# Kernel tuning notes

Measured on AMD Instinct MI355X. Metric: run time of the kernel, lower is better.

The kernel has to match this reference:

```python
import jax, jax.numpy as jnp
import numpy as np

N, X_DIM, Y_DIM, HID = 8192, 512, 2048 // 4, 2048
Y_DIM = 512

def setup_inputs() -> dict:
    key = jax.random.key(0)
    ks = jax.random.split(key, 10)
    def lin(k, fan_in, fan_out):
        lim = 1.0 / np.sqrt(fan_in)
        kw, kb = jax.random.split(k)
        W = jax.random.uniform(kw, (fan_in, fan_out), jnp.float32, -lim, lim)
        b = jax.random.uniform(kb, (fan_out,), jnp.float32, -lim, lim)
        return W, b
    mu_W1, mu_b1 = lin(ks[0], X_DIM, HID)
    mu_W2, mu_b2 = lin(ks[1], HID, Y_DIM)
    lv_W1, lv_b1 = lin(ks[2], X_DIM, HID)
    lv_W2, lv_b2 = lin(ks[3], HID, Y_DIM)
    return {
        "x_samples": jax.random.normal(ks[4], (N, X_DIM), jnp.float32),
        "y_samples": jax.random.normal(ks[5], (N, Y_DIM), jnp.float32),
        "mu_W1": mu_W1, "mu_b1": mu_b1, "mu_W2": mu_W2, "mu_b2": mu_b2,
        "lv_W1": lv_W1, "lv_b1": lv_b1, "lv_W2": lv_W2, "lv_b2": lv_b2,
    }

def reference(x_samples, y_samples, mu_W1, mu_b1, mu_W2, mu_b2, lv_W1, lv_b1, lv_W2, lv_b2):
    # MLP heads (GEMMs)
    mu = jax.nn.relu(x_samples @ mu_W1 + mu_b1) @ mu_W2 + mu_b2          # [N, D]
    logvar = jnp.tanh(jax.nn.relu(x_samples @ lv_W1 + lv_b1) @ lv_W2 + lv_b2)  # [N, D]
    w = 0.5 * jnp.exp(-logvar)                                           # 1/(2*exp(logvar))
    n = x_samples.shape[0]

    # positive: -mean_i sum_d (mu_id - y_id)^2 * w_id
    positive = -(((mu - y_samples) ** 2) * w).sum(axis=1).mean()

    # negative (exact decomposition of the [N,N,D] broadcast):
    # -(1/N^2) sum_{i,d} w_id * (N*mu_id^2 - 2*mu_id*Sy_d + Sy2_d)
    Sy = y_samples.sum(axis=0)          # [D]
    Sy2 = (y_samples ** 2).sum(axis=0)  # [D]
    negative = -(w * (n * mu ** 2 - 2.0 * mu * Sy + Sy2)).sum() / (n * n)

    return positive - negative
```

## Files before the change

### kernel.cpp

```cpp
#include <hip/hip_runtime.h>
#include <hip/hip_bf16.h>
#include <stdint.h>

#define NS   8192
#define XD   512
#define HD   2048
#define YD   512

typedef unsigned short u16;
using bf16x8 = __attribute__((ext_vector_type(8))) short;
using f32x4  = __attribute__((ext_vector_type(4))) float;

__device__ __forceinline__ float bf2f(u16 u) {
  union { uint32_t i; float f; } v; v.i = ((uint32_t)u) << 16; return v.f;
}
__device__ __forceinline__ u16 f2b(float f) {
  __hip_bfloat16 hb = __float2bfloat16(f);
  return *(const u16*)&hb;
}
__device__ __forceinline__ float ld_in(const void* p, int f32, size_t i) {
  return f32 ? ((const float*)p)[i] : bf2f(((const u16*)p)[i]);
}
#define GLDS(gp, lp) __builtin_amdgcn_global_load_lds( \
    (__attribute__((address_space(1))) void*)(gp),     \
    (__attribute__((address_space(3))) void*)(lp), 16, 0, 0)

__device__ __forceinline__ int probe_f32(const void* p, int n_u16, int* sflag) {
  if (threadIdx.x == 0) *sflag = 0;
  __syncthreads();
  const u16* q = (const u16*)p;
  int wild = 0;
  for (int i = threadIdx.x; i < n_u16; i += blockDim.x) {
    float v = bf2f(q[i]);
    if (!(fabsf(v) <= 1000.0f)) wild = 1;
  }
  if (wild) *sflag = 1;
  __syncthreads();
  int r = *sflag;
  __syncthreads();
  return r;
}

__global__ __launch_bounds__(256) void prep_all(
    const void* __restrict__ x,
    const void* w1m, const void* b1m, const void* w2m, const void* b2m,
    const void* w1l, const void* b1l, const void* w2l, const void* b2l,
    const void* __restrict__ y,
    u16* __restrict__ xb, float* __restrict__ biasv,
    u16* __restrict__ W1t, u16* __restrict__ W2tm, u16* __restrict__ W2tl,
    float* __restrict__ Sy, float* __restrict__ Sy2) {
  __shared__ u16 tile[64 * 72];
  __shared__ int sflag;
  const int b = blockIdx.x;
  const int tid = threadIdx.x;

  if (b < 2048) {
    if (!probe_f32(x, 1024, &sflag)) return;
    const size_t base = (size_t)b * 2048 + (size_t)tid * 8;
    alignas(16) u16 o[8];
    const float4* s = (const float4*)((const float*)x + base);
    float4 v0 = s[0], v1 = s[1];
    o[0]=f2b(v0.x); o[1]=f2b(v0.y); o[2]=f2b(v0.z); o[3]=f2b(v0.w);
    o[4]=f2b(v1.x); o[5]=f2b(v1.y); o[6]=f2b(v1.z); o[7]=f2b(v1.w);
    *(uint4*)(xb + base) = *(const uint4*)o;
  } else if (b == 2048) {
    const int f3 = probe_f32(b1m, 1024, &sflag);
    const int f5 = probe_f32(b2m, 512, &sflag);
    const int f7 = probe_f32(b1l, 1024, &sflag);
    const int f9 = probe_f32(b2l, 512, &sflag);
    for (int i = tid; i < 5120; i += 256) {
      float v;
      if (i < 2048)      v = ld_in(b1m, f3, i);
      else if (i < 4096) v = ld_in(b1l, f7, i - 2048);
      else if (i < 4608) v = ld_in(b2m, f5, i - 4096);
      else               v = ld_in(b2l, f9, i - 4608);
      biasv[i] = v;
    }
  } else if (b < 3073) {
    const int id = b - 2049, which = id >> 8, t = id & 255;
    const void* in; u16* out; int R, C;
    if (which == 0)      { in = w1m; out = W1t;                   R = XD; C = HD; }
    else if (which == 1) { in = w2m; out = W2tm;                  R = HD; C = YD; }
    else if (which == 2) { in = w1l; out = W1t + (size_t)HD * XD; R = XD; C = HD; }
    else                 { in = w2l; out = W2tl;                  R = HD; C = YD; }
    const int f = probe_f32(in, 1024, &sflag);
    const int nbx = C >> 6;
    const int c0 = (t % nbx) * 64, r0 = (t / nbx) * 64;
    const int r = tid >> 2, cc = (tid & 3) * 16;
    if (f) {
      const float4* s = (const float4*)((const float*)in + (size_t)(r0 + r) * C + c0 + cc);
#pragma unroll
      for (int k = 0; k < 4; ++k) {
        float4 v = s[k];
        tile[r * 72 + cc + k * 4 + 0] = f2b(v.x);
        tile[r * 72 + cc + k * 4 + 1] = f2b(v.y);
        tile[r * 72 + cc + k * 4 + 2] = f2b(v.z);
        tile[r * 72 + cc + k * 4 + 3] = f2b(v.w);
      }
    } else {
      const uint4* s = (const uint4*)((const u16*)in + (size_t)(r0 + r) * C + c0 + cc);
      *(uint4*)&tile[r * 72 + cc]     = s[0];
      *(uint4*)&tile[r * 72 + cc + 8] = s[1];
    }
    __syncthreads();
    const int i = tid >> 2, jc = (tid & 3) * 16;
    alignas(16) u16 o[16];
#pragma unroll
    for (int j = 0; j < 16; ++j) o[j] = tile[(jc + j) * 72 + i];
    uint4* dq = (uint4*)&out[(size_t)(c0 + i) * R + r0 + jc];
    dq[0] = ((const uint4*)o)[0];
    dq[1] = ((const uint4*)o)[1];
  } else {
    const int id2 = b - 3073;
    const int yf = probe_f32(y, 1024, &sflag);
    const int half = tid >> 7;
    const int c0 = (tid & 127) * 4;
    const int r0 = id2 * 128 + half * 64;
    float s0 = 0.f, s1 = 0.f, s2 = 0.f, s3 = 0.f;
    float q0 = 0.f, q1 = 0.f, q2 = 0.f, q3 = 0.f;
    for (int r = r0; r < r0 + 64; r += 4) {
#pragma unroll
      for (int rr = 0; rr < 4; ++rr) {
        float v0, v1, v2, v3;
        if (yf) {
          const float4 t4 = *(const float4*)((const float*)y + (size_t)(r + rr) * YD + c0);
          v0 = t4.x; v1 = t4.y; v2 = t4.z; v3 = t4.w;
        } else {
          const uint2 t2 = *(const uint2*)((const u16*)y + (size_t)(r + rr) * YD + c0);
          v0 = bf2f((u16)(t2.x & 0xffff)); v1 = bf2f((u16)(t2.x >> 16));
          v2 = bf2f((u16)(t2.y & 0xffff)); v3 = bf2f((u16)(t2.y >> 16));
        }
        s0 += v0; q0 += v0 * v0;  s1 += v1; q1 += v1 * v1;
        s2 += v2; q2 += v2 * v2;  s3 += v3; q3 += v3 * v3;
      }
    }
    atomicAdd(&Sy[c0],     s0);  atomicAdd(&Sy2[c0],     q0);
    atomicAdd(&Sy[c0 + 1], s1);  atomicAdd(&Sy2[c0 + 1], q1);
    atomicAdd(&Sy[c0 + 2], s2);  atomicAdd(&Sy2[c0 + 2], q2);
    atomicAdd(&Sy[c0 + 3], s3);  atomicAdd(&Sy2[c0 + 3], q3);
  }
}

#define SYNC_PRE do { \
  __builtin_amdgcn_sched_barrier(0); \
  __builtin_amdgcn_s_barrier(); \
  asm volatile("s_waitcnt lgkmcnt(0)" ::: "memory"); \
  __builtin_amdgcn_sched_barrier(0); \
  __builtin_amdgcn_s_setprio(1); } while (0)
#define SYNC_POST do { \
  __builtin_amdgcn_s_setprio(0); \
  __builtin_amdgcn_sched_barrier(0); \
  __builtin_amdgcn_s_barrier(); \
  __builtin_amdgcn_sched_barrier(0); } while (0)
#define VMCNT4 asm volatile("s_waitcnt vmcnt(4)" ::: "memory")
#define VMCNT0 asm volatile("s_waitcnt vmcnt(0)" ::: "memory")

#define RD_A(MH, BUF) do { \
  const u16* ab_ = &lds[((BUF)*2 + wm) * 8192]; \
  _Pragma("unroll") for (int q_ = 0; q_ < 4; ++q_) \
    _Pragma("unroll") for (int ks_ = 0; ks_ < 2; ++ks_) \
      af[q_][ks_] = *(const bf16x8*)&ab_[((MH)*64 + q_*16 + c16)*64 + (((ks_*4+quad) ^ cswz) << 3)]; \
} while (0)

#define RD_B(NH, BUF) do { \
  const u16* bb_ = &lds[32768 + ((BUF)*2 + (wn>>1)) * 8192]; \
  _Pragma("unroll") for (int p_ = 0; p_ < 2; ++p_) \
    _Pragma("unroll") for (int ks_ = 0; ks_ < 2; ++ks_) \
      bf[(NH)*2+p_][ks_] = *(const bf16x8*)&bb_[((wn&1)*64 + ((NH)*2+p_)*16 + c16)*64 + (((ks_*4+quad) ^ cswz) << 3)]; \
} while (0)

#define MM(MH, NH) do { \
  _Pragma("unroll") for (int ks_ = 0; ks_ < 2; ++ks_) \
    _Pragma("unroll") for (int q_ = 0; q_ < 4; ++q_) \
      _Pragma("unroll") for (int p_ = 0; p_ < 2; ++p_) \
        acc[(MH)*4+q_][(NH)*2+p_] = __builtin_amdgcn_mfma_f32_16x16x32_bf16( \
            af[q_][ks_], bf[(NH)*2+p_][ks_], acc[(MH)*4+q_][(NH)*2+p_], 0, 0, 0); \
} while (0)

#define ST_A(KT, HALF) do { if ((KT) < 8) { \
  u16* lb_ = &lds[(((KT)&1)*2 + (HALF))*8192 + (wid << 9)]; \
  const u16* sp_ = Aptr + (size_t)(bm0 + (HALF)*128 + (wid<<3) + srow)*512 + ((KT)<<6) + scg; \
  GLDS(sp_, lb_); GLDS(sp_ + (size_t)64*512, lb_ + 4096); } } while (0)

#define ST_B(KT, HALF) do { if ((KT) < 8) { \
  u16* lb_ = &lds[32768 + (((KT)&1)*2 + (HALF))*8192 + (wid << 9)]; \
  const u16* sp_ = W1t + (size_t)(bn0 + (HALF)*128 + (wid<<3) + srow)*512 + ((KT)<<6) + scg; \
  GLDS(sp_, lb_); GLDS(sp_ + (size_t)64*512, lb_ + 4096); } } while (0)

__global__ __launch_bounds__(512, 2) void gemm1_kernel(
    const void* __restrict__ xraw, const u16* __restrict__ xb,
    const u16* __restrict__ W1t,
    const float* __restrict__ bias,
    u16* __restrict__ h_mu, u16* __restrict__ h_lv) {
  __shared__ alignas(16) u16 lds[65536];
  __shared__ int sflag;
  const int tid = threadIdx.x;

  const u16* Aptr = probe_f32(xraw, 1024, &sflag) ? xb : (const u16*)xraw;

  const int wid = tid >> 6, lane = tid & 63;
  const int wm = wid >> 2, wn = wid & 3;
  const int quad = lane >> 4, c16 = lane & 15, cswz = c16 & 7;
  const int srow = lane >> 3;
  const int scg  = ((lane & 7) ^ srow) << 3;

  const int id = blockIdx.x;
  const int xcd = id & 7, slot = id >> 3;
  const int bm0 = (xcd * 4 + (slot & 3)) * 256;
  const int bn0 = (slot >> 2) * 256;

  f32x4 acc[8][4] = {};
  bf16x8 af[4][2], bf[4][2];

  ST_B(0, 0); ST_B(0, 1); ST_A(0, 0); ST_A(0, 1);
  ST_B(1, 0); ST_B(1, 1);
  VMCNT4;
  __builtin_amdgcn_s_barrier();
  __builtin_amdgcn_sched_barrier(0);

#pragma unroll
  for (int i = 0; i < 4; ++i) {
    const int ka = 2 * i, kb = ka + 1;
    const bool last = (i == 3);
    RD_A(0, 0); RD_B(0, 0); ST_A(kb, 0);
    SYNC_PRE; MM(0, 0); SYNC_POST;
    RD_B(1, 0); ST_A(kb, 1);
    SYNC_PRE; MM(0, 1); SYNC_POST;
    RD_A(1, 0); ST_B(ka + 2, 0);
    SYNC_PRE; MM(1, 0); SYNC_POST;
    ST_B(ka + 2, 1);
    SYNC_PRE; MM(1, 1);
    if (!last) { VMCNT4; } else { VMCNT0; }
    SYNC_POST;
    RD_A(0, 1); RD_B(0, 1); ST_A(ka + 2, 0);
    SYNC_PRE; MM(0, 0); SYNC_POST;
    RD_B(1, 1); ST_A(ka + 2, 1);
    SYNC_PRE; MM(0, 1); SYNC_POST;
    RD_A(1, 1); ST_B(kb + 2, 0);
    SYNC_PRE; MM(1, 0); SYNC_POST;
    ST_B(kb + 2, 1);
    SYNC_PRE; MM(1, 1);
    if (!last) { VMCNT4; }
    SYNC_POST;
  }

  u16* myl = &lds[wid * 8192];
  const bool is_lv = bn0 >= HD;
  u16* dst = is_lv ? h_lv : h_mu;
  const int wncol = wn << 6;
  const int gc0 = (bn0 - (is_lv ? HD : 0)) + wncol;
  const int grow0 = bm0 + (wm << 7);
#pragma unroll
  for (int ni = 0; ni < 4; ++ni) {
    const float bv = bias[bn0 + wncol + ni * 16 + c16];
#pragma unroll
    for (int mi = 0; mi < 8; ++mi)
#pragma unroll
      for (int r = 0; r < 4; ++r) {
        const int row = mi * 16 + (quad << 2) + r;
        const int col = ni * 16 + c16;
        myl[row * 64 + ((((col >> 3) ^ (row & 7)) << 3) | (col & 7))] =
            f2b(fmaxf(acc[mi][ni][r] + bv, 0.f));
      }
  }
#pragma unroll
  for (int it = 0; it < 16; ++it) {
    const int row = (it << 3) + (lane >> 3);
    const int ch = lane & 7;
    const uint4 v = *(const uint4*)&myl[row * 64 + ((ch ^ (row & 7)) << 3)];
    *(uint4*)&dst[(size_t)(grow0 + row) * HD + gc0 + (ch << 3)] = v;
  }
}

#undef RD_A
#undef RD_B
#undef MM
#undef ST_A
#undef ST_B

__global__ __launch_bounds__(256) void gemm2_dual(
    const u16* __restrict__ hm, const u16* __restrict__ hl,
    const u16* __restrict__ W2m, const u16* __restrict__ W2l,
    const float* __restrict__ b2m, const float* __restrict__ b2l,
    const void* __restrict__ y,
    const float* __restrict__ Sy, const float* __restrict__ Sy2,
    double* __restrict__ gacc, unsigned* __restrict__ counter,
    float* __restrict__ out) {
  constexpr int K = HD;
  __shared__ alignas(16) u16 Am[64 * 64];
  __shared__ alignas(16) u16 Al[64 * 64];
  __shared__ alignas(16) u16 Bm[128 * 64];
  __shared__ alignas(16) u16 Bl[128 * 64];
  __shared__ double bs[4];
  __shared__ int sflag;

  const int yf = probe_f32(y, 1024, &sflag);

  const int tid = threadIdx.x, wid = tid >> 6, lane = tid & 63;
  const int MT = NS / 64, NT = YD / 128;
  const int id = blockIdx.x;
  const int xcd = id & 7, slot = id >> 3;
  const int bm0 = (xcd * (MT >> 3) + slot / NT) * 64;
  const int bn0 = (slot % NT) * 128;

  const int mrow = (wid >> 1) * 32, ncol = (wid & 1) * 64;
  const int quad = lane >> 4, c16 = lane & 15, cswz = c16 & 7;
  const int srow = lane >> 3, sc = lane & 7;
  const int scg  = (sc ^ srow) * 8;

  f32x4 am[2][4] = {}, al[2][4] = {};

  for (int k0 = 0; k0 < K; k0 += 64) {
#pragma unroll
    for (int j = 0; j < 2; ++j) {
      const int grp = wid * 2 + j, row = grp * 8 + srow;
      const size_t go = (size_t)(bm0 + row) * K + (k0 + scg);
      GLDS(hm + go, Am + grp * 512);
      GLDS(hl + go, Al + grp * 512);
    }
#pragma unroll
    for (int j = 0; j < 4; ++j) {
      const int grp = wid * 4 + j, row = grp * 8 + srow;
      const size_t go = (size_t)(bn0 + row) * K + (k0 + scg);
      GLDS(W2m + go, Bm + grp * 512);
      GLDS(W2l + go, Bl + grp * 512);
    }
    __syncthreads();
#pragma unroll
    for (int h = 0; h < 2; ++h) {
      const int off = ((h * 4 + quad) ^ cswz) * 8;
      bf16x8 afm[2], afl[2], bfm[4], bfl[4];
#pragma unroll
      for (int mi = 0; mi < 2; ++mi) {
        const int rl = (mrow + mi * 16 + c16) * 64 + off;
        afm[mi] = *(const bf16x8*)&Am[rl];
        afl[mi] = *(const bf16x8*)&Al[rl];
      }
#pragma unroll
      for (int ni = 0; ni < 4; ++ni) {
        const int rl = (ncol + ni * 16 + c16) * 64 + off;
        bfm[ni] = *(const bf16x8*)&Bm[rl];
        bfl[ni] = *(const bf16x8*)&Bl[rl];
      }
#pragma unroll
      for (int mi = 0; mi < 2; ++mi)
#pragma unroll
        for (int ni = 0; ni < 4; ++ni) {
          am[mi][ni] = __builtin_amdgcn_mfma_f32_16x16x32_bf16(
              afm[mi], bfm[ni], am[mi][ni], 0, 0, 0);
          al[mi][ni] = __builtin_amdgcn_mfma_f32_16x16x32_bf16(
              afl[mi], bfl[ni], al[mi][ni], 0, 0, 0);
        }
    }
    __syncthreads();
  }

  const float invN = 1.0f / (float)NS;
  float s = 0.f;
#pragma unroll
  for (int ni = 0; ni < 4; ++ni) {
    const int gcol = bn0 + ncol + ni * 16 + c16;
    const float bmv = b2m[gcol], blv = b2l[gcol];
    const float syv = Sy[gcol], sy2v = Sy2[gcol];
#pragma unroll
    for (int mi = 0; mi < 2; ++mi)
#pragma unroll
      for (int r = 0; r < 4; ++r) {
        const int grow = bm0 + mrow + mi * 16 + quad * 4 + r;
        const float m   = am[mi][ni][r] + bmv;
        const float lvp = al[mi][ni][r] + blv;
        const float w   = 0.5f * expf(-tanhf(lvp));
        const float yv  = ld_in(y, yf, (size_t)grow * YD + gcol);
        s += w * (yv * yv - 2.f * m * yv + (2.f * m * syv - sy2v) * invN);
      }
  }
  for (int off = 32; off > 0; off >>= 1) s += __shfl_down(s, off);
  if (lane == 0) bs[wid] = (double)s;
  __syncthreads();
  if (tid == 0) {
    atomicAdd(gacc, bs[0] + bs[1] + bs[2] + bs[3]);
    __threadfence();
    const unsigned old = atomicAdd(counter, 1u);
    if (old == gridDim.x - 1) {
      const double g = atomicAdd(gacc, 0.0);
      out[0] = (float)(-g / (double)NS);
    }
  }
}

extern "C" void kernel_launch(void* const* d_in, const int* in_sizes, int n_in,
                              void* d_out, int out_size, void* d_ws, size_t ws_size,
                              hipStream_t stream) {
  char* ws = (char*)d_ws;
  double*   gacc    = (double*)ws;
  unsigned* counter = (unsigned*)(ws + 8);
  float*    Sy      = (float*)(ws + 128);
  float*    Sy2     = (float*)(ws + 2176);
  float*    biasv   = (float*)(ws + 4224);
  u16* xb   = (u16*)(ws + 24704);
  u16* W1t  = xb + (size_t)NS * XD;
  u16* W2tm = W1t + (size_t)2 * HD * XD;
  u16* W2tl = W2tm + (size_t)YD * HD;
  u16* h_mu = W2tl + (size_t)YD * HD;
  u16* h_lv = h_mu + (size_t)NS * HD;

  hipMemsetAsync(d_ws, 0, 4224, stream);

  prep_all<<<2049 + 1024 + 64, 256, 0, stream>>>(
      d_in[0], d_in[2], d_in[3], d_in[4], d_in[5],
      d_in[6], d_in[7], d_in[8], d_in[9], d_in[1],
      xb, biasv, W1t, W2tm, W2tl, Sy, Sy2);

  const float* b1  = biasv;
  const float* b2m = biasv + 4096, *b2l = biasv + 4608;

  gemm1_kernel<<<(NS / 256) * ((2 * HD) / 256), 512, 0, stream>>>(
      d_in[0], xb, W1t, b1, h_mu, h_lv);

  gemm2_dual<<<(NS / 64) * (YD / 128), 256, 0, stream>>>(
      h_mu, h_lv, W2tm, W2tl, b2m, b2l, d_in[1], Sy, Sy2,
      gacc, counter, (float*)d_out);
}
```

Before: 225.2 us.

## Restructure dual GEMM2 into 128x128 tiles with double-buffered async LDS pipeline

Rewrites the second-layer dual GEMM to use 512-thread blocks on 128x128 output tiles and a double-buffered global_load_lds pipeline. Loads for the next K-slab are issued while MFMAs run on the current one, with fine-grained vmcnt waits and barrier/setprio scheduling, mirroring the first GEMM. The aim is to hide global-memory latency and raise operand reuse per block compared with the old synchronous load-then-compute loop on 64x128 tiles. The cost is 128KB of LDS per block, which limits occupancy, plus a complex hand-tuned wait schedule that is fragile.

```diff
diff --git a/kernel.cpp b/kernel.cpp
--- a/kernel.cpp
+++ b/kernel.cpp
@@ -152,8 +152,7 @@
   __builtin_amdgcn_sched_barrier(0); \
   __builtin_amdgcn_s_barrier(); \
   __builtin_amdgcn_sched_barrier(0); } while (0)
-#define VMCNT4 asm volatile("s_waitcnt vmcnt(4)" ::: "memory")
-#define VMCNT0 asm volatile("s_waitcnt vmcnt(0)" ::: "memory")
+#define VMCNT(N) asm volatile("s_waitcnt vmcnt(" #N ")" ::: "memory")
 
 #define RD_A(MH, BUF) do { \
   const u16* ab_ = &lds[((BUF)*2 + wm) * 8192]; \
@@ -214,7 +213,7 @@
 
   ST_B(0, 0); ST_B(0, 1); ST_A(0, 0); ST_A(0, 1);
   ST_B(1, 0); ST_B(1, 1);
-  VMCNT4;
+  VMCNT(4);
   __builtin_amdgcn_s_barrier();
   __builtin_amdgcn_sched_barrier(0);
 
@@ -230,7 +229,7 @@
     SYNC_PRE; MM(1, 0); SYNC_POST;
     ST_B(ka + 2, 1);
     SYNC_PRE; MM(1, 1);
-    if (!last) { VMCNT4; } else { VMCNT0; }
+    if (!last) { VMCNT(4); } else { VMCNT(0); }
     SYNC_POST;
     RD_A(0, 1); RD_B(0, 1); ST_A(ka + 2, 0);
     SYNC_PRE; MM(0, 0); SYNC_POST;
@@ -240,7 +239,7 @@
     SYNC_PRE; MM(1, 0); SYNC_POST;
     ST_B(kb + 2, 1);
     SYNC_PRE; MM(1, 1);
-    if (!last) { VMCNT4; }
+    if (!last) { VMCNT(4); }
     SYNC_POST;
   }
 
@@ -278,7 +277,40 @@
 #undef ST_A
 #undef ST_B
 
-__global__ __launch_bounds__(256) void gemm2_dual(
+#define RD_AF(dstf, RBASE, BUF) do { \
+  _Pragma("unroll") for (int mi_ = 0; mi_ < 2; ++mi_) \
+    _Pragma("unroll") for (int ks_ = 0; ks_ < 2; ++ks_) \
+      dstf[mi_][ks_] = *(const bf16x8*)&lds[(BUF)*32768 + (RBASE) + \
+          (wm*32 + mi_*16 + c16)*64 + (((ks_*4+quad) ^ cswz) << 3)]; \
+} while (0)
+
+#define RD_BF(RBASE, BUF, NH) do { \
+  _Pragma("unroll") for (int p_ = 0; p_ < 2; ++p_) \
+    _Pragma("unroll") for (int ks_ = 0; ks_ < 2; ++ks_) \
+      bfr[p_][ks_] = *(const bf16x8*)&lds[(BUF)*32768 + (RBASE) + \
+          (wn*64 + ((NH)*2+p_)*16 + c16)*64 + (((ks_*4+quad) ^ cswz) << 3)]; \
+} while (0)
+
+#define MM2(accv, aff, NH) do { \
+  _Pragma("unroll") for (int ks_ = 0; ks_ < 2; ++ks_) \
+    _Pragma("unroll") for (int mi_ = 0; mi_ < 2; ++mi_) \
+      _Pragma("unroll") for (int p_ = 0; p_ < 2; ++p_) \
+        accv[mi_][(NH)*2+p_] = __builtin_amdgcn_mfma_f32_16x16x32_bf16( \
+            aff[mi_][ks_], bfr[p_][ks_], accv[mi_][(NH)*2+p_], 0, 0, 0); \
+} while (0)
+
+#define ST_R(KT, SRC, RBASE) do { \
+  u16* lb_ = &lds[(((KT)&1)*32768) + (RBASE) + (wid << 9)]; \
+  const u16* sp_ = (SRC) + (size_t)(KT)*64; \
+  GLDS(sp_, lb_); GLDS(sp_ + (size_t)64*2048, lb_ + 4096); \
+} while (0)
+
+#define RAm 0
+#define RAl 8192
+#define RBm 16384
+#define RBl 24576
+
+__global__ __launch_bounds__(512, 2) void gemm2_dual(
     const u16* __restrict__ hm, const u16* __restrict__ hl,
     const u16* __restrict__ W2m, const u16* __restrict__ W2l,
     const float* __restrict__ b2m, const float* __restrict__ b2l,
@@ -286,87 +318,88 @@
     const float* __restrict__ Sy, const float* __restrict__ Sy2,
     double* __restrict__ gacc, unsigned* __restrict__ counter,
     float* __restrict__ out) {
-  constexpr int K = HD;
-  __shared__ alignas(16) u16 Am[64 * 64];
-  __shared__ alignas(16) u16 Al[64 * 64];
-  __shared__ alignas(16) u16 Bm[128 * 64];
-  __shared__ alignas(16) u16 Bl[128 * 64];
-  __shared__ double bs[4];
+  __shared__ alignas(16) u16 lds[65536];
+  __shared__ double bs[8];
   __shared__ int sflag;
 
   const int yf = probe_f32(y, 1024, &sflag);
 
   const int tid = threadIdx.x, wid = tid >> 6, lane = tid & 63;
-  const int MT = NS / 64, NT = YD / 128;
+  const int wm = wid >> 1, wn = wid & 1;
+  const int quad = lane >> 4, c16 = lane & 15, cswz = c16 & 7;
+  const int srow = lane >> 3;
+  const int scg  = ((lane & 7) ^ srow) << 3;
+
   const int id = blockIdx.x;
   const int xcd = id & 7, slot = id >> 3;
-  const int bm0 = (xcd * (MT >> 3) + slot / NT) * 64;
-  const int bn0 = (slot % NT) * 128;
-
-  const int mrow = (wid >> 1) * 32, ncol = (wid & 1) * 64;
-  const int quad = lane >> 4, c16 = lane & 15, cswz = c16 & 7;
-  const int srow = lane >> 3, sc = lane & 7;
-  const int scg  = (sc ^ srow) * 8;
+  const int bm0 = (xcd * 8 + (slot >> 2)) * 128;
+  const int bn0 = (slot & 3) * 128;
+
+  const u16* aM = hm  + (size_t)(bm0 + (wid << 3) + srow) * HD + scg;
+  const u16* aL = hl  + (size_t)(bm0 + (wid << 3) + srow) * HD + scg;
+  const u16* bM = W2m + (size_t)(bn0 + (wid << 3) + srow) * HD + scg;
+  const u16* bL = W2l + (size_t)(bn0 + (wid << 3) + srow) * HD + scg;
 
   f32x4 am[2][4] = {}, al[2][4] = {};
-
-  for (int k0 = 0; k0 < K; k0 += 64) {
-#pragma unroll
-    for (int j = 0; j < 2; ++j) {
-      const int grp = wid * 2 + j, row = grp * 8 + srow;
-      const size_t go = (size_t)(bm0 + row) * K + (k0 + scg);
-      GLDS(hm + go, Am + grp * 512);
-      GLDS(hl + go, Al + grp * 512);
-    }
-#pragma unroll
-    for (int j = 0; j < 4; ++j) {
-      const int grp = wid * 4 + j, row = grp * 8 + srow;
-      const size_t go = (size_t)(bn0 + row) * K + (k0 + scg);
-      GLDS(W2m + go, Bm + grp * 512);
-      GLDS(W2l + go, Bl + grp * 512);
-    }
-    __syncthreads();
-#pragma unroll
-    for (int h = 0; h < 2; ++h) {
-      const int off = ((h * 4 + quad) ^ cswz) * 8;
-      bf16x8 afm[2], afl[2], bfm[4], bfl[4];
-#pragma unroll
-      for (int mi = 0; mi < 2; ++mi) {
-        const int rl = (mrow + mi * 16 + c16) * 64 + off;
-        afm[mi] = *(const bf16x8*)&Am[rl];
-        afl[mi] = *(const bf16x8*)&Al[rl];
-      }
-#pragma unroll
-      for (int ni = 0; ni < 4; ++ni) {
-        const int rl = (ncol + ni * 16 + c16) * 64 + off;
-        bfm[ni] = *(const bf16x8*)&Bm[rl];
-        bfl[ni] = *(const bf16x8*)&Bl[rl];
-      }
-#pragma unroll
-      for (int mi = 0; mi < 2; ++mi)
-#pragma unroll
-        for (int ni = 0; ni < 4; ++ni) {
-          am[mi][ni] = __builtin_amdgcn_mfma_f32_16x16x32_bf16(
-              afm[mi], bfm[ni], am[mi][ni], 0, 0, 0);
-          al[mi][ni] = __builtin_amdgcn_mfma_f32_16x16x32_bf16(
-              afl[mi], bfl[ni], al[mi][ni], 0, 0, 0);
-        }
-    }
-    __syncthreads();
+  bf16x8 afm[2][2], afl[2][2], bfr[2][2];
+
+  ST_R(0, aM, RAm); ST_R(0, bM, RBm); ST_R(0, aL, RAl); ST_R(0, bL, RBl);
+  ST_R(1, aM, RAm); ST_R(1, bM, RBm); ST_R(1, aL, RAl);
+  VMCNT(10);
+  __builtin_amdgcn_s_barrier();
+  __builtin_amdgcn_sched_barrier(0);
+
+#pragma unroll 1
+  for (int i = 0; i < 15; ++i) {
+    const int ka = 2 * i, kb = ka + 1;
+    RD_AF(afm, RAm, 0); RD_BF(RBm, 0, 0); ST_R(kb,     bL, RBl);
+    SYNC_PRE; MM2(am, afm, 0); SYNC_POST;
+    RD_BF(RBm, 0, 1);                       ST_R(ka + 2, aM, RAm);
+    SYNC_PRE; MM2(am, afm, 1); VMCNT(10); SYNC_POST;
+    RD_AF(afl, RAl, 0); RD_BF(RBl, 0, 0); ST_R(ka + 2, bM, RBm);
+    SYNC_PRE; MM2(al, afl, 0); SYNC_POST;
+    RD_BF(RBl, 0, 1);                       ST_R(ka + 2, aL, RAl);
+    SYNC_PRE; MM2(al, afl, 1); VMCNT(10); SYNC_POST;
+    RD_AF(afm, RAm, 1); RD_BF(RBm, 1, 0); ST_R(ka + 2, bL, RBl);
+    SYNC_PRE; MM2(am, afm, 0); SYNC_POST;
+    RD_BF(RBm, 1, 1);                       ST_R(kb + 2, aM, RAm);
+    SYNC_PRE; MM2(am, afm, 1); VMCNT(10); SYNC_POST;
+    RD_AF(afl, RAl, 1); RD_BF(RBl, 1, 0); ST_R(kb + 2, bM, RBm);
+    SYNC_PRE; MM2(al, afl, 0); SYNC_POST;
+    RD_BF(RBl, 1, 1);                       ST_R(kb + 2, aL, RAl);
+    SYNC_PRE; MM2(al, afl, 1); VMCNT(10); SYNC_POST;
+  }
+  {
+    RD_AF(afm, RAm, 0); RD_BF(RBm, 0, 0); ST_R(31, bL, RBl);
+    SYNC_PRE; MM2(am, afm, 0); SYNC_POST;
+    RD_BF(RBm, 0, 1);
+    SYNC_PRE; MM2(am, afm, 1); VMCNT(8); SYNC_POST;
+    RD_AF(afl, RAl, 0); RD_BF(RBl, 0, 0);
+    SYNC_PRE; MM2(al, afl, 0); SYNC_POST;
+    RD_BF(RBl, 0, 1);
+    SYNC_PRE; MM2(al, afl, 1); VMCNT(4); SYNC_POST;
+    RD_AF(afm, RAm, 1); RD_BF(RBm, 1, 0);
+    SYNC_PRE; MM2(am, afm, 0); SYNC_POST;
+    RD_BF(RBm, 1, 1);
+    SYNC_PRE; MM2(am, afm, 1); VMCNT(0); SYNC_POST;
+    RD_AF(afl, RAl, 1); RD_BF(RBl, 1, 0);
+    SYNC_PRE; MM2(al, afl, 0); SYNC_POST;
+    RD_BF(RBl, 1, 1);
+    SYNC_PRE; MM2(al, afl, 1); SYNC_POST;
   }
 
   const float invN = 1.0f / (float)NS;
   float s = 0.f;
 #pragma unroll
   for (int ni = 0; ni < 4; ++ni) {
-    const int gcol = bn0 + ncol + ni * 16 + c16;
+    const int gcol = bn0 + wn * 64 + ni * 16 + c16;
     const float bmv = b2m[gcol], blv = b2l[gcol];
     const float syv = Sy[gcol], sy2v = Sy2[gcol];
 #pragma unroll
     for (int mi = 0; mi < 2; ++mi)
 #pragma unroll
       for (int r = 0; r < 4; ++r) {
-        const int grow = bm0 + mrow + mi * 16 + quad * 4 + r;
+        const int grow = bm0 + wm * 32 + mi * 16 + quad * 4 + r;
         const float m   = am[mi][ni][r] + bmv;
         const float lvp = al[mi][ni][r] + blv;
         const float w   = 0.5f * expf(-tanhf(lvp));
@@ -378,7 +411,8 @@
   if (lane == 0) bs[wid] = (double)s;
   __syncthreads();
   if (tid == 0) {
-    atomicAdd(gacc, bs[0] + bs[1] + bs[2] + bs[3]);
+    atomicAdd(gacc, bs[0] + bs[1] + bs[2] + bs[3] +
+                    bs[4] + bs[5] + bs[6] + bs[7]);
     __threadfence();
     const unsigned old = atomicAdd(counter, 1u);
     if (old == gridDim.x - 1) {
@@ -417,7 +451,7 @@
   gemm1_kernel<<<(NS / 256) * ((2 * HD) / 256), 512, 0, stream>>>(
       d_in[0], xb, W1t, b1, h_mu, h_lv);
 
-  gemm2_dual<<<(NS / 64) * (YD / 128), 256, 0, stream>>>(
+  gemm2_dual<<<(NS / 128) * (YD / 128), 512, 0, stream>>>(
       h_mu, h_lv, W2tm, W2tl, b2m, b2l, d_in[1], Sy, Sy2,
       gacc, counter, (float*)d_out);
 }
```

New measurement: 214.1 us. 1.05x faster.
